# Kernel tuning notes

Measured on AMD Instinct MI355X. Metric: run time of the kernel, lower is better.

Reference implementation:

```python
import jax, jax.numpy as jnp
import numpy as np

# Static problem sizes (uniform T/taus make the ragged edge list static).
B, N, F, T, TAU, S = 8, 384, 64, 192, 192, 5
SINK_SHIFT = T                    # min sink index == T (sinks are the new nodes)
N_SINK, N_SOURCE = TAU, T + TAU - 1


def _edge_indices():
    # tril_indices(T+tau, offset=-1), keep sink >= T  (window=None)
    r, c = np.tril_indices(T + TAU, k=-1)
    m = r >= T
    r, c = r[m], c[m]
    e = r.shape[0]
    batch = np.repeat(np.arange(B), e)
    return (jnp.asarray(batch, jnp.int32),
            jnp.asarray(np.tile(r, B), jnp.int32),
            jnp.asarray(np.tile(c, B), jnp.int32))


def setup_inputs() -> dict:
    key = jax.random.key(0)
    ks = jax.random.split(key, 6)
    batch_idx, sink_idx, source_idx = _edge_indices()
    s1, s2 = 1.0 / np.sqrt(2 * F), 1.0 / np.sqrt(F)
    return {
        "nodes": jax.random.normal(ks[0], (B, N, F), jnp.float32),
        "w1": jax.random.uniform(ks[1], (2 * F, F), jnp.float32, -s1, s1),
        "b1": jnp.zeros((F,), jnp.float32),
        "g1": jnp.ones((F,), jnp.float32),
        "be1": jnp.zeros((F,), jnp.float32),
        "w2": jax.random.uniform(ks[2], (F, F), jnp.float32, -s2, s2),
        "b2": jnp.zeros((F,), jnp.float32),
        "g2": jnp.ones((F,), jnp.float32),
        "be2": jnp.zeros((F,), jnp.float32),
        "w3": jax.random.uniform(ks[3], (F, 1), jnp.float32, -s2, s2),
        "b3": jnp.zeros((1,), jnp.float32),
        "gumbel": jax.random.gumbel(ks[4], (S, B, N_SINK, N_SOURCE), jnp.float32),
        "batch_idx": batch_idx,
        "sink_idx": sink_idx,
        "source_idx": source_idx,
    }


def _ln(x, g, b):
    mu = x.mean(-1, keepdims=True)
    v = ((x - mu) ** 2).mean(-1, keepdims=True)
    return (x - mu) * jax.lax.rsqrt(v + 1e-5) * g + b


def reference(nodes, w1, b1, g1, be1, w2, b2, g2, be2, w3, b3,
              gumbel, batch_idx, sink_idx, source_idx):
    # gather sink/source node pairs: [E, 2F]
    sink = nodes[batch_idx, sink_idx]
    src = nodes[batch_idx, source_idx]
    x = jnp.concatenate([sink, src], axis=-1)
    # edge MLP -> per-edge logit
    h = _ln(jax.nn.relu(x @ w1 + b1), g1, be1)
    h = _ln(jax.nn.relu(h @ w2 + b2), g2, be2)
    logits = (h @ w3 + b3)[:, 0]                     # [E]
    # dense-padded grid filled with finfo.min (as in torch)
    neg = jnp.finfo(jnp.float32).min
    gs = jnp.full((B, N_SINK, N_SOURCE), neg, jnp.float32)
    gs = gs.at[batch_idx, sink_idx - SINK_SHIFT, source_idx].set(logits)
    # hard gumbel-softmax over source dim, S independent samples
    y_soft = jax.nn.softmax(gs[None] + gumbel, axis=-1)      # [S,B,192,383]
    y_hard = jax.nn.one_hot(jnp.argmax(y_soft, -1), N_SOURCE, dtype=y_soft.dtype)
    y = y_soft + jax.lax.stop_gradient(y_hard - y_soft)
    e = y.sum(0)
    # straight-through binarize: forward (e>0), backward identity
    e = e + jax.lax.stop_gradient((e > 0).astype(e.dtype) - e)
    valid = e[batch_idx, sink_idx - SINK_SHIFT, source_idx]
    vals = jnp.where(valid > 0, valid, 0.0)
    # dense equivalent of the sparse COO adjacency (B, N, N)
    return jnp.zeros((B, N, N), jnp.float32).at[batch_idx, sink_idx, source_idx].set(vals)
```

## Files before the change

### kernel.cpp

```cpp
#include <hip/hip_runtime.h>
#include <math.h>
#include <stdint.h>

#define BB 8
#define NN 384
#define FF 64
#define TT 192
#define NSRC 383
#define NSINK 192
#define SS 5
#define NEDGE 441600
#define BN (BB * NN)
#define TILE_E 256
#define NBLKE (NEDGE / TILE_E)
#define OUTV ((BB * NN * NN) / 4)

typedef _Float16 half8 __attribute__((ext_vector_type(8)));
typedef __fp16 fp16x2 __attribute__((ext_vector_type(2)));
typedef float floatx4 __attribute__((ext_vector_type(4)));
typedef uint32_t uint4v __attribute__((ext_vector_type(4)));

static __device__ __forceinline__ void split_f16(float x, uint16_t& h, uint16_t& l) {
  const _Float16 hh = (_Float16)x;
  const float hb = (float)hh;
  const _Float16 ll = (_Float16)((x - hb) * 512.f);
  h = __builtin_bit_cast(uint16_t, hh);
  l = __builtin_bit_cast(uint16_t, ll);
}

static __device__ __forceinline__ void split_pair(float x0, float x1,
                                                  uint32_t& hi, uint32_t& lo) {
  const fp16x2 h = __builtin_amdgcn_cvt_pkrtz(x0, x1);
  const float hb0 = (float)h.x, hb1 = (float)h.y;
  const fp16x2 l = __builtin_amdgcn_cvt_pkrtz((x0 - hb0) * 512.f, (x1 - hb1) * 512.f);
  hi = __builtin_bit_cast(uint32_t, h);
  lo = __builtin_bit_cast(uint32_t, l);
}

__global__ __launch_bounds__(64) void prep_all(
    const float* __restrict__ nodes, const float* __restrict__ w1,
    const float* __restrict__ b1,
    const float* __restrict__ w2, const float* __restrict__ b2,
    const float* __restrict__ g1, const float* __restrict__ be1,
    const float* __restrict__ g2, const float* __restrict__ be2,
    const float* __restrict__ w3, const float* __restrict__ b3,
    float* __restrict__ A, float* __restrict__ Bv,
    unsigned short* __restrict__ Whg, unsigned short* __restrict__ Wlg,
    float* __restrict__ wcol, float* __restrict__ cb,
    float* __restrict__ gw, float* __restrict__ cwsgw) {
  const int blk = blockIdx.x;
  const int k = threadIdx.x;
  if (blk < BN / 4) {
    const int bn0 = blk * 4;
    __shared__ float nd[4][FF];
#pragma unroll
    for (int i = 0; i < 4; ++i) nd[i][k] = nodes[(bn0 + i) * FF + k];
    __syncthreads();
    const float bk = b1[k];
    float a0 = bk, a1 = bk, a2 = bk, a3 = bk;
    float q0 = 0.f, q1 = 0.f, q2 = 0.f, q3 = 0.f;
#pragma unroll 8
    for (int f = 0; f < FF; ++f) {
      const float wt = w1[f * FF + k];
      const float wb = w1[(FF + f) * FF + k];
      const float n0 = nd[0][f], n1 = nd[1][f], n2 = nd[2][f], n3 = nd[3][f];
      a0 = fmaf(n0, wt, a0); a1 = fmaf(n1, wt, a1);
      a2 = fmaf(n2, wt, a2); a3 = fmaf(n3, wt, a3);
      q0 = fmaf(n0, wb, q0); q1 = fmaf(n1, wb, q1);
      q2 = fmaf(n2, wb, q2); q3 = fmaf(n3, wb, q3);
    }
    A[(bn0 + 0) * FF + k] = a0;
    A[(bn0 + 1) * FF + k] = a1;
    A[(bn0 + 2) * FF + k] = a2;
    A[(bn0 + 3) * FF + k] = a3;
    const int f4 = k >> 2, ff = k & 3;
    Bv[(f4 * BN + (bn0 + 0)) * 4 + ff] = q0;
    Bv[(f4 * BN + (bn0 + 1)) * 4 + ff] = q1;
    Bv[(f4 * BN + (bn0 + 2)) * 4 + ff] = q2;
    Bv[(f4 * BN + (bn0 + 3)) * 4 + ff] = q3;
  } else {
    const int j = k;
    const int jt = j >> 4, m = j & 15;
    float cbj = b2[j];
    float wc = 0.f;
    for (int kk = 0; kk < FF; ++kk) {
      const float wraw = w2[kk * FF + j];
      const float w = g1[kk] * wraw;
      wc += w;
      cbj = fmaf(be1[kk], wraw, cbj);
      uint16_t hu, lu;
      split_f16(w, hu, lu);
      const int kc = kk >> 5, qq = (kk >> 3) & 3, jj = kk & 7;
      const int idx = (((jt * 2 + kc) * 4 + qq) * 16 + m) * 8 + jj;
      Whg[idx] = hu;
      Wlg[idx] = lu;
    }
    wcol[j] = wc;
    cb[j] = cbj;
    const float gwj = g2[j] * w3[j];
    gw[j] = gwj;
    __shared__ float sA[FF], sB[FF];
    sA[j] = gwj;
    sB[j] = be2[j] * w3[j];
    __syncthreads();
    if (j == 0) {
      float a = 0.f, bq = 0.f;
      for (int i = 0; i < FF; ++i) { a += sA[i]; bq += sB[i]; }
      cwsgw[0] = b3[0] + bq;
      cwsgw[1] = a;
    }
  }
}

__global__ __launch_bounds__(256, 3) void edge_mlp(
    const float* __restrict__ A, const float* __restrict__ Bv,
    const unsigned short* __restrict__ Whg, const unsigned short* __restrict__ Wlg,
    const float* __restrict__ wcolg, const float* __restrict__ cbg,
    const float* __restrict__ gwg, const float* __restrict__ cwsgw,
    const int* __restrict__ bidx, const int* __restrict__ ridx,
    const int* __restrict__ cidx, float* __restrict__ L,
    float4* __restrict__ outv) {
  __shared__ __align__(16) unsigned short WhS[4096];
  __shared__ __align__(16) unsigned short WlS[4096];

  const int tid = threadIdx.x;
  const int lane = tid & 63;
  const int q = lane >> 4;
  const int n = lane & 15;

  {
    const int4* gh = (const int4*)Whg;
    const int4* gl = (const int4*)Wlg;
    int4* sh = (int4*)WhS;
    int4* sl = (int4*)WlS;
    sh[tid] = gh[tid];
    sh[tid + 256] = gh[tid + 256];
    sl[tid] = gl[tid];
    sl[tid + 256] = gl[tid + 256];
  }

  const int gtid = blockIdx.x * 256 + tid;
  if (gtid < OUTV) outv[gtid] = make_float4(0.f, 0.f, 0.f, 0.f);

  const int ebase = blockIdx.x * TILE_E + (tid >> 6) * 64 + n;
  int eb[4], er[4], ec[4];
#pragma unroll
  for (int et = 0; et < 4; ++et) {
    eb[et] = bidx[ebase + 16 * et];
    er[et] = ridx[ebase + 16 * et];
    ec[et] = cidx[ebase + 16 * et];
  }
  const float cw = cwsgw[0], sgw = cwsgw[1];
  const float4* __restrict__ pb4 = (const float4*)Bv;

  __syncthreads();

#pragma unroll
  for (int et = 0; et < 4; ++et) {
    const int b = eb[et], r = er[et], c = ec[et];
    const float4* pa = (const float4*)(A + (b * NN + r) * FF);
    const int colB = b * NN + c;
    const float4 a0 = pa[2 * q],     a1 = pa[2 * q + 1];
    const float4 a2 = pa[8 + 2 * q], a3 = pa[8 + 2 * q + 1];
    const float4 v0 = pb4[(2 * q) * BN + colB];
    const float4 v1 = pb4[(2 * q + 1) * BN + colB];
    const float4 v2 = pb4[(8 + 2 * q) * BN + colB];
    const float4 v3 = pb4[(8 + 2 * q + 1) * BN + colB];

    const float x0 = fmaxf(a0.x + v0.x, 0.f);
    const float x1 = fmaxf(a0.y + v0.y, 0.f);
    const float x2 = fmaxf(a0.z + v0.z, 0.f);
    const float x3 = fmaxf(a0.w + v0.w, 0.f);
    const float x4 = fmaxf(a1.x + v1.x, 0.f);
    const float x5 = fmaxf(a1.y + v1.y, 0.f);
    const float x6 = fmaxf(a1.z + v1.z, 0.f);
    const float x7 = fmaxf(a1.w + v1.w, 0.f);
    const float x8 = fmaxf(a2.x + v2.x, 0.f);
    const float x9 = fmaxf(a2.y + v2.y, 0.f);
    const float x10 = fmaxf(a2.z + v2.z, 0.f);
    const float x11 = fmaxf(a2.w + v2.w, 0.f);
    const float x12 = fmaxf(a3.x + v3.x, 0.f);
    const float x13 = fmaxf(a3.y + v3.y, 0.f);
    const float x14 = fmaxf(a3.z + v3.z, 0.f);
    const float x15 = fmaxf(a3.w + v3.w, 0.f);

    uint32_t h0, l0, h1, l1, h2, l2, h3, l3;
    split_pair(x0, x1, h0, l0); split_pair(x2, x3, h1, l1);
    split_pair(x4, x5, h2, l2); split_pair(x6, x7, h3, l3);
    const uint4v hv0 = {h0, h1, h2, h3}, lv0 = {l0, l1, l2, l3};
    const half8 xh0 = __builtin_bit_cast(half8, hv0);
    const half8 xl0 = __builtin_bit_cast(half8, lv0);
    split_pair(x8, x9, h0, l0);  split_pair(x10, x11, h1, l1);
    split_pair(x12, x13, h2, l2); split_pair(x14, x15, h3, l3);
    const uint4v hv1 = {h0, h1, h2, h3}, lv1 = {l0, l1, l2, l3};
    const half8 xh1 = __builtin_bit_cast(half8, hv1);
    const half8 xl1 = __builtin_bit_cast(half8, lv1);

    float s = x0 + x1 + x2 + x3 + x4 + x5 + x6 + x7 +
              x8 + x9 + x10 + x11 + x12 + x13 + x14 + x15;
    float qa = 0.f;
    qa = fmaf(x0, x0, qa); qa = fmaf(x1, x1, qa);
    qa = fmaf(x2, x2, qa); qa = fmaf(x3, x3, qa);
    qa = fmaf(x4, x4, qa); qa = fmaf(x5, x5, qa);
    qa = fmaf(x6, x6, qa); qa = fmaf(x7, x7, qa);
    qa = fmaf(x8, x8, qa); qa = fmaf(x9, x9, qa);
    qa = fmaf(x10, x10, qa); qa = fmaf(x11, x11, qa);
    qa = fmaf(x12, x12, qa); qa = fmaf(x13, x13, qa);
    qa = fmaf(x14, x14, qa); qa = fmaf(x15, x15, qa);
    s += __shfl_xor(s, 16, 64);  s += __shfl_xor(s, 32, 64);
    qa += __shfl_xor(qa, 16, 64); qa += __shfl_xor(qa, 32, 64);
    const float mu = s * (1.f / FF);
    const float rstd = 1.f / sqrtf(qa * (1.f / FF) - mu * mu + 1e-5f);

    floatx4 acc0[4], acc1[4];
#pragma unroll
    for (int jt = 0; jt < 4; ++jt) {
      acc0[jt] = (floatx4){0.f, 0.f, 0.f, 0.f};
      acc1[jt] = (floatx4){0.f, 0.f, 0.f, 0.f};
    }
#pragma unroll
    for (int kc = 0; kc < 2; ++kc) {
      const half8 xh = kc ? xh1 : xh0;
      const half8 xl = kc ? xl1 : xl0;
#pragma unroll
      for (int jt = 0; jt < 4; ++jt) {
        const int woff = (((jt * 2 + kc) * 4 + q) * 16 + n) * 8;
        const half8 wh = *(const half8*)&WhS[woff];
        const half8 wl = *(const half8*)&WlS[woff];
        acc0[jt] = __builtin_amdgcn_mfma_f32_16x16x32_f16(wh, xh, acc0[jt], 0, 0, 0);
        acc1[jt] = __builtin_amdgcn_mfma_f32_16x16x32_f16(wh, xl, acc1[jt], 0, 0, 0);
        acc1[jt] = __builtin_amdgcn_mfma_f32_16x16x32_f16(wl, xh, acc1[jt], 0, 0, 0);
      }
    }

    float s1 = 0.f, sq2 = 0.f, s3 = 0.f;
#pragma unroll
    for (int jt = 0; jt < 4; ++jt) {
      const floatx4 wc4 = *(const floatx4*)(wcolg + 16 * jt + 4 * q);
      const floatx4 cb4 = *(const floatx4*)(cbg + 16 * jt + 4 * q);
      const floatx4 gw4 = *(const floatx4*)(gwg + 16 * jt + 4 * q);
      const floatx4 t4 = acc0[jt] + acc1[jt] * (1.f / 512.f);
#pragma unroll
      for (int rg = 0; rg < 4; ++rg) {
        const float pre = fmaf(rstd, fmaf(-mu, wc4[rg], t4[rg]), cb4[rg]);
        const float tr = fmaxf(pre, 0.f);
        s1 += tr;
        sq2 = fmaf(tr, tr, sq2);
        s3 = fmaf(tr, gw4[rg], s3);
      }
    }
    s1 += __shfl_xor(s1, 16, 64);  s1 += __shfl_xor(s1, 32, 64);
    sq2 += __shfl_xor(sq2, 16, 64); sq2 += __shfl_xor(sq2, 32, 64);
    s3 += __shfl_xor(s3, 16, 64);  s3 += __shfl_xor(s3, 32, 64);
    if (q == 0) {
      const float mu2 = s1 * (1.f / FF);
      const float var2 = sq2 * (1.f / FF) - mu2 * mu2;
      const float rstd2 = 1.f / sqrtf(var2 + 1e-5f);
      const float logit = fmaf(rstd2, fmaf(-mu2, sgw, s3), cw);
      L[(b * NSINK + (r - TT)) * NSRC + c] = logit;
    }
  }
}

__global__ __launch_bounds__(256) void argmax_scatter(
    const float* __restrict__ L, const float* __restrict__ gum,
    float* __restrict__ out) {
  const int pair = blockIdx.x * 4 + (threadIdx.x >> 6);
  const int lane = threadIdx.x & 63;
  const int row = pair % NSINK;
  const int b = pair / NSINK;
  const int r = row + TT;

  const float* __restrict__ lrow = L + (b * NSINK + row) * NSRC;
  const float* __restrict__ g0 = gum + (b * NSINK + row) * NSRC;
  const int sstr = BB * NSINK * NSRC;

  float bv0 = -INFINITY, bv1 = -INFINITY, bv2 = -INFINITY, bv3 = -INFINITY, bv4 = -INFINITY;
  int bi0 = 0, bi1 = 0, bi2 = 0, bi3 = 0, bi4 = 0;
  for (int cc = lane; cc < r; cc += 64) {
    const float lv = lrow[cc];
    const float v0 = lv + g0[0 * sstr + cc];
    const float v1 = lv + g0[1 * sstr + cc];
    const float v2 = lv + g0[2 * sstr + cc];
    const float v3 = lv + g0[3 * sstr + cc];
    const float v4 = lv + g0[4 * sstr + cc];
    if (v0 > bv0) { bv0 = v0; bi0 = cc; }
    if (v1 > bv1) { bv1 = v1; bi1 = cc; }
    if (v2 > bv2) { bv2 = v2; bi2 = cc; }
    if (v3 > bv3) { bv3 = v3; bi3 = cc; }
    if (v4 > bv4) { bv4 = v4; bi4 = cc; }
  }
#pragma unroll
  for (int off = 32; off > 0; off >>= 1) {
    {
      const float ov = __shfl_xor(bv0, off, 64); const int oi = __shfl_xor(bi0, off, 64);
      if (ov > bv0 || (ov == bv0 && oi < bi0)) { bv0 = ov; bi0 = oi; }
    }
    {
      const float ov = __shfl_xor(bv1, off, 64); const int oi = __shfl_xor(bi1, off, 64);
      if (ov > bv1 || (ov == bv1 && oi < bi1)) { bv1 = ov; bi1 = oi; }
    }
    {
      const float ov = __shfl_xor(bv2, off, 64); const int oi = __shfl_xor(bi2, off, 64);
      if (ov > bv2 || (ov == bv2 && oi < bi2)) { bv2 = ov; bi2 = oi; }
    }
    {
      const float ov = __shfl_xor(bv3, off, 64); const int oi = __shfl_xor(bi3, off, 64);
      if (ov > bv3 || (ov == bv3 && oi < bi3)) { bv3 = ov; bi3 = oi; }
    }
    {
      const float ov = __shfl_xor(bv4, off, 64); const int oi = __shfl_xor(bi4, off, 64);
      if (ov > bv4 || (ov == bv4 && oi < bi4)) { bv4 = ov; bi4 = oi; }
    }
  }
  if (lane == 0) {
    float* __restrict__ orow = out + (b * NN + r) * NN;
    orow[bi0] = 1.0f;
    orow[bi1] = 1.0f;
    orow[bi2] = 1.0f;
    orow[bi3] = 1.0f;
    orow[bi4] = 1.0f;
  }
}

extern "C" void kernel_launch(void* const* d_in, const int* in_sizes, int n_in,
                              void* d_out, int out_size, void* d_ws, size_t ws_size,
                              hipStream_t stream) {
  const float* nodes = (const float*)d_in[0];
  const float* w1 = (const float*)d_in[1];
  const float* b1 = (const float*)d_in[2];
  const float* g1 = (const float*)d_in[3];
  const float* be1 = (const float*)d_in[4];
  const float* w2 = (const float*)d_in[5];
  const float* b2 = (const float*)d_in[6];
  const float* g2 = (const float*)d_in[7];
  const float* be2 = (const float*)d_in[8];
  const float* w3 = (const float*)d_in[9];
  const float* b3 = (const float*)d_in[10];
  const float* gum = (const float*)d_in[11];
  const int* bidx = (const int*)d_in[12];
  const int* ridx = (const int*)d_in[13];
  const int* cidx = (const int*)d_in[14];
  float* out = (float*)d_out;

  float* ws = (float*)d_ws;
  float* A = ws;
  float* Bv = A + BN * FF;
  unsigned short* Whg = (unsigned short*)(ws + 393216);
  unsigned short* Wlg = Whg + 4096;
  float* wcol = ws + 397312;
  float* cb = wcol + FF;
  float* gw = cb + FF;
  float* cwsgw = gw + FF;
  float* L = ws + 397520;
  (void)ws_size; (void)n_in; (void)in_sizes; (void)out_size;

  hipLaunchKernelGGL(prep_all, dim3(BN / 4 + 1), dim3(64), 0, stream,
                     nodes, w1, b1, w2, b2, g1, be1, g2, be2, w3, b3,
                     A, Bv, Whg, Wlg, wcol, cb, gw, cwsgw);
  hipLaunchKernelGGL(edge_mlp, dim3(NBLKE), dim3(256), 0, stream,
                     A, Bv, Whg, Wlg, wcol, cb, gw, cwsgw, bidx, ridx, cidx, L,
                     (float4*)out);
  hipLaunchKernelGGL(argmax_scatter, dim3((BB * NSINK) / 4), dim3(256), 0, stream,
                     L, gum, out);
}
```

Baseline: 132.1 us.

## Replace per-edge index gathers with per-sink-row task table and prefetch

Instead of reading batch/sink/source index arrays per edge, a task table built in prep_all maps each wave to a (batch, sink row, 64-column chunk). This lets each wave load its sink-side A row once and stream contiguous source columns, prefetching the next column group's Bv values while computing the current one. Per-column LN constants move to shared memory. The cost is padded lanes at row ends, masked by c<r, and a few more tasks than with exact edge tiling.

```diff
diff --git a/kernel.cpp b/kernel.cpp
--- a/kernel.cpp
+++ b/kernel.cpp
@@ -11,9 +11,10 @@
 #define SS 5
 #define NEDGE 441600
 #define BN (BB * NN)
-#define TILE_E 256
-#define NBLKE (NEDGE / TILE_E)
 #define OUTV ((BB * NN * NN) / 4)
+#define TPB_TASK 957
+#define NTASK (BB * TPB_TASK)
+#define NBLK_T (NTASK / 4)
 
 typedef _Float16 half8 __attribute__((ext_vector_type(8)));
 typedef __fp16 fp16x2 __attribute__((ext_vector_type(2)));
@@ -47,7 +48,8 @@
     float* __restrict__ A, float* __restrict__ Bv,
     unsigned short* __restrict__ Whg, unsigned short* __restrict__ Wlg,
     float* __restrict__ wcol, float* __restrict__ cb,
-    float* __restrict__ gw, float* __restrict__ cwsgw) {
+    float* __restrict__ gw, float* __restrict__ cwsgw,
+    int2* __restrict__ tab) {
   const int blk = blockIdx.x;
   const int k = threadIdx.x;
   if (blk < BN / 4) {
@@ -78,7 +80,7 @@
     Bv[(f4 * BN + (bn0 + 1)) * 4 + ff] = q1;
     Bv[(f4 * BN + (bn0 + 2)) * 4 + ff] = q2;
     Bv[(f4 * BN + (bn0 + 3)) * 4 + ff] = q3;
-  } else {
+  } else if (blk == BN / 4) {
     const int j = k;
     const int jt = j >> 4, m = j & 15;
     float cbj = b2[j];
@@ -109,6 +111,19 @@
       cwsgw[0] = b3[0] + bq;
       cwsgw[1] = a;
     }
+  } else {
+    for (int rr = k; rr < NSINK; rr += 64) {
+      const int r = TT + rr;
+      int tb;
+      if (r == 192) tb = 0;
+      else if (r < 257) tb = 3 + 4 * (r - 193);
+      else if (r < 321) tb = 259 + 5 * (r - 257);
+      else tb = 579 + 6 * (r - 321);
+      const int nt = (r + 63) >> 6;
+      for (int b = 0; b < BB; ++b)
+        for (int i = 0; i < nt; ++i)
+          tab[b * TPB_TASK + tb + i] = make_int2((r << 16) | (i * 64), b);
+    }
   }
 }
 
@@ -117,13 +132,14 @@
     const unsigned short* __restrict__ Whg, const unsigned short* __restrict__ Wlg,
     const float* __restrict__ wcolg, const float* __restrict__ cbg,
     const float* __restrict__ gwg, const float* __restrict__ cwsgw,
-    const int* __restrict__ bidx, const int* __restrict__ ridx,
-    const int* __restrict__ cidx, float* __restrict__ L,
+    const int2* __restrict__ tab, float* __restrict__ L,
     float4* __restrict__ outv) {
   __shared__ __align__(16) unsigned short WhS[4096];
   __shared__ __align__(16) unsigned short WlS[4096];
+  __shared__ __align__(16) float wcolS[FF], cbS[FF], gwS[FF];
 
   const int tid = threadIdx.x;
+  const int wave = tid >> 6;
   const int lane = tid & 63;
   const int q = lane >> 4;
   const int n = lane & 15;
@@ -137,35 +153,45 @@
     sh[tid + 256] = gh[tid + 256];
     sl[tid] = gl[tid];
     sl[tid + 256] = gl[tid + 256];
+    if (tid < FF) {
+      wcolS[tid] = wcolg[tid];
+      cbS[tid] = cbg[tid];
+      gwS[tid] = gwg[tid];
+    }
   }
 
   const int gtid = blockIdx.x * 256 + tid;
   if (gtid < OUTV) outv[gtid] = make_float4(0.f, 0.f, 0.f, 0.f);
 
-  const int ebase = blockIdx.x * TILE_E + (tid >> 6) * 64 + n;
-  int eb[4], er[4], ec[4];
+  const int2 d = tab[blockIdx.x * 4 + wave];
+  const int r = d.x >> 16;
+  const int c0 = d.x & 0xffff;
+  const int b = d.y;
+  const float cw = cwsgw[0], sgw = cwsgw[1];
+
+  const float4* pa = (const float4*)(A + (b * NN + r) * FF);
+  const float4 a0 = pa[2 * q], a1 = pa[2 * q + 1];
+  const float4 a2 = pa[8 + 2 * q], a3 = pa[8 + 2 * q + 1];
+  const float4* __restrict__ pb4 = (const float4*)Bv;
+  const int colbase = b * NN + c0 + n;
+
+  __syncthreads();
+
+  float4 v0 = pb4[(2 * q) * BN + colbase];
+  float4 v1 = pb4[(2 * q + 1) * BN + colbase];
+  float4 v2 = pb4[(8 + 2 * q) * BN + colbase];
+  float4 v3 = pb4[(8 + 2 * q + 1) * BN + colbase];
+
 #pragma unroll
   for (int et = 0; et < 4; ++et) {
-    eb[et] = bidx[ebase + 16 * et];
-    er[et] = ridx[ebase + 16 * et];
-    ec[et] = cidx[ebase + 16 * et];
-  }
-  const float cw = cwsgw[0], sgw = cwsgw[1];
-  const float4* __restrict__ pb4 = (const float4*)Bv;
-
-  __syncthreads();
-
-#pragma unroll
-  for (int et = 0; et < 4; ++et) {
-    const int b = eb[et], r = er[et], c = ec[et];
-    const float4* pa = (const float4*)(A + (b * NN + r) * FF);
-    const int colB = b * NN + c;
-    const float4 a0 = pa[2 * q],     a1 = pa[2 * q + 1];
-    const float4 a2 = pa[8 + 2 * q], a3 = pa[8 + 2 * q + 1];
-    const float4 v0 = pb4[(2 * q) * BN + colB];
-    const float4 v1 = pb4[(2 * q + 1) * BN + colB];
-    const float4 v2 = pb4[(8 + 2 * q) * BN + colB];
-    const float4 v3 = pb4[(8 + 2 * q + 1) * BN + colB];
+    float4 nv0, nv1, nv2, nv3;
+    if (et < 3) {
+      const int cnx = colbase + 16 * (et + 1);
+      nv0 = pb4[(2 * q) * BN + cnx];
+      nv1 = pb4[(2 * q + 1) * BN + cnx];
+      nv2 = pb4[(8 + 2 * q) * BN + cnx];
+      nv3 = pb4[(8 + 2 * q + 1) * BN + cnx];
+    }
 
     const float x0 = fmaxf(a0.x + v0.x, 0.f);
     const float x1 = fmaxf(a0.y + v0.y, 0.f);
@@ -236,9 +262,9 @@
     float s1 = 0.f, sq2 = 0.f, s3 = 0.f;
 #pragma unroll
     for (int jt = 0; jt < 4; ++jt) {
-      const floatx4 wc4 = *(const floatx4*)(wcolg + 16 * jt + 4 * q);
-      const floatx4 cb4 = *(const floatx4*)(cbg + 16 * jt + 4 * q);
-      const floatx4 gw4 = *(const floatx4*)(gwg + 16 * jt + 4 * q);
+      const floatx4 wc4 = *(const floatx4*)&wcolS[16 * jt + 4 * q];
+      const floatx4 cb4 = *(const floatx4*)&cbS[16 * jt + 4 * q];
+      const floatx4 gw4 = *(const floatx4*)&gwS[16 * jt + 4 * q];
       const floatx4 t4 = acc0[jt] + acc1[jt] * (1.f / 512.f);
 #pragma unroll
       for (int rg = 0; rg < 4; ++rg) {
@@ -252,13 +278,16 @@
     s1 += __shfl_xor(s1, 16, 64);  s1 += __shfl_xor(s1, 32, 64);
     sq2 += __shfl_xor(sq2, 16, 64); sq2 += __shfl_xor(sq2, 32, 64);
     s3 += __shfl_xor(s3, 16, 64);  s3 += __shfl_xor(s3, 32, 64);
-    if (q == 0) {
+    const int c2 = c0 + 16 * et + n;
+    if (q == 0 && c2 < r) {
       const float mu2 = s1 * (1.f / FF);
       const float var2 = sq2 * (1.f / FF) - mu2 * mu2;
       const float rstd2 = 1.f / sqrtf(var2 + 1e-5f);
       const float logit = fmaf(rstd2, fmaf(-mu2, sgw, s3), cw);
-      L[(b * NSINK + (r - TT)) * NSRC + c] = logit;
-    }
+      L[(b * NSINK + (r - TT)) * NSRC + c2] = logit;
+    }
+
+    if (et < 3) { v0 = nv0; v1 = nv1; v2 = nv2; v3 = nv3; }
   }
 }
 
@@ -338,9 +367,6 @@
   const float* w3 = (const float*)d_in[9];
   const float* b3 = (const float*)d_in[10];
   const float* gum = (const float*)d_in[11];
-  const int* bidx = (const int*)d_in[12];
-  const int* ridx = (const int*)d_in[13];
-  const int* cidx = (const int*)d_in[14];
   float* out = (float*)d_out;
 
   float* ws = (float*)d_ws;
@@ -353,13 +379,14 @@
   float* gw = cb + FF;
   float* cwsgw = gw + FF;
   float* L = ws + 397520;
+  int2* tab = (int2*)(ws + 985808);
   (void)ws_size; (void)n_in; (void)in_sizes; (void)out_size;
 
-  hipLaunchKernelGGL(prep_all, dim3(BN / 4 + 1), dim3(64), 0, stream,
+  hipLaunchKernelGGL(prep_all, dim3(BN / 4 + 2), dim3(64), 0, stream,
                      nodes, w1, b1, w2, b2, g1, be1, g2, be2, w3, b3,
-                     A, Bv, Whg, Wlg, wcol, cb, gw, cwsgw);
-  hipLaunchKernelGGL(edge_mlp, dim3(NBLKE), dim3(256), 0, stream,
-                     A, Bv, Whg, Wlg, wcol, cb, gw, cwsgw, bidx, ridx, cidx, L,
+                     A, Bv, Whg, Wlg, wcol, cb, gw, cwsgw, tab);
+  hipLaunchKernelGGL(edge_mlp, dim3(NBLK_T), dim3(256), 0, stream,
+                     A, Bv, Whg, Wlg, wcol, cb, gw, cwsgw, tab, L,
                      (float4*)out);
   hipLaunchKernelGGL(argmax_scatter, dim3((BB * NSINK) / 4), dim3(256), 0, stream,
                      L, gum, out);
```

New measurement: 129.1 us. -2.3%, faster.
